# Kernel tuning notes

Hardware: AMD Instinct MI355X
Metric: run time of the kernel (lower is better)

Reference implementation:

```python
import jax, jax.numpy as jnp
import numpy as np

B, H, N, P = 2, 8, 2048, 64   # batch, heads, seq, head_dim
M, D = 4, 256                 # sketch count, sketch feature dim


def setup_inputs() -> dict:
    key = jax.random.key(0)
    kq, kk, ks, kr = jax.random.split(key, 4)
    scale = P ** -0.5  # keep exp(QK) numerically tame, std(dot) ~= 1/8
    Q = jax.random.normal(kq, (B, H, N, P), dtype=jnp.float32) * scale
    K = jax.random.normal(kk, (B, H, N, P), dtype=jnp.float32) * scale
    # indices into the concatenated [Q;K] token axis of length 2N
    sketching_matrix = jax.random.randint(ks, (B, M, D), 0, 2 * N)
    # Rademacher random signs, broadcast over [b,h,2n] in the reduction
    random_sign = jnp.sign(jax.random.normal(kr, (M, D), dtype=jnp.float32))
    random_sign = jnp.where(random_sign == 0, 1.0, random_sign)
    return {"Q": Q, "K": K, "sketching_matrix": sketching_matrix,
            "random_sign": random_sign}


def reference(Q, K, sketching_matrix, random_sign):
    b, h, n, p = Q.shape
    X = jnp.concatenate([Q, K], axis=2)          # [b,h,2n,p]
    Xt = jnp.transpose(X, (0, 2, 1, 3))          # [b,2n,h,p]
    # gather sketched landmarks: [b,m,d,h,p] -> [b,h,m,d,p]
    XS = Xt[jnp.arange(b)[:, None, None], sketching_matrix]
    XS = jnp.transpose(XS, (0, 3, 1, 2, 4))
    # RS_SM accumulate branch: exp of inner products, random-sign reduce over m
    product = jnp.einsum('bhnp,bhmdp->bhnmd', X, XS)   # [b,h,2n,m,d]
    AS = jnp.einsum('bhnmd,md->bhnd', jnp.exp(product), random_sign)
    return AS.astype(Q.dtype)                    # [b,h,2n,d]
```

## Files before the change

kernel.cpp:

```cpp
#include <hip/hip_runtime.h>
#include <hip/hip_bf16.h>

typedef __attribute__((ext_vector_type(8))) short short8;
typedef __attribute__((ext_vector_type(4))) float f32x4;

namespace {
constexpr int Nc  = 2048;
constexpr int NXc = 4096;
constexpr int Pc  = 64;
constexpr int Mc  = 4;
constexpr int Dc  = 256;
constexpr int BH  = 16;
constexpr int LDW = 72;
constexpr float LOG2E = 1.4426950408889634f;
}

__device__ inline float fexp2(float x) {
#if __has_builtin(__builtin_amdgcn_exp2f)
  return __builtin_amdgcn_exp2f(x);
#else
  return exp2f(x);
#endif
}

__device__ inline unsigned int bfpack(float a, float b) {
  union { __hip_bfloat162 h; unsigned int u; } cv;
  cv.h = __float22bfloat162_rn(make_float2(a, b));
  return cv.u;
}

__global__ __launch_bounds__(256) void prepass_kernel(
    const float* __restrict__ Q, const float* __restrict__ K,
    const int* __restrict__ SK, __hip_bfloat16* __restrict__ Wb)
{
  const int t  = blockIdx.x * 256 + threadIdx.x;
  const int q  = t & 7;
  const int r  = t >> 3;
  const int bh = r >> 10;
  const int md = r & 1023;
  const int b  = bh >> 3;
  const int idx = SK[b * (Mc * Dc) + md];
  const float* src = (idx < Nc) ? (Q + ((size_t)bh * Nc + idx) * Pc)
                                : (K + ((size_t)bh * Nc + (idx - Nc)) * Pc);
  const f32x4* s4 = (const f32x4*)(src + q * 8);
  f32x4 f0 = s4[0], f1 = s4[1];
  uint4 u;
  u.x = bfpack(f0.x * LOG2E, f0.y * LOG2E);
  u.y = bfpack(f0.z * LOG2E, f0.w * LOG2E);
  u.z = bfpack(f1.x * LOG2E, f1.y * LOG2E);
  u.w = bfpack(f1.z * LOG2E, f1.w * LOG2E);
  *(uint4*)(Wb + (size_t)r * Pc + q * 8) = u;
}

__global__ __launch_bounds__(256, 4) void sketch_main(
    const float* __restrict__ Q, const float* __restrict__ K,
    const __hip_bfloat16* __restrict__ Wb,
    const float* __restrict__ SGN, float* __restrict__ OUT)
{
  __shared__ __hip_bfloat16 Ws[2][64][LDW];
  __shared__ float Ss[Mc * Dc];

  const int t    = threadIdx.x;
  const int lane = t & 63;
  const int wv   = t >> 6;
  const int brow = lane & 15;
  const int q    = lane >> 4;
  const int bh   = blockIdx.y;
  const int n0   = blockIdx.x * 64;

  for (int i = t; i < Mc * Dc; i += 256) Ss[i] = SGN[i];

  const int nrow = n0 + wv * 16 + brow;
  const float* xsrc = (n0 < Nc) ? (Q + ((size_t)bh * Nc + nrow) * Pc)
                                : (K + ((size_t)bh * Nc + (nrow - Nc)) * Pc);
  f32x4 x0 = *(const f32x4*)(xsrc + q * 8);
  f32x4 x1 = *(const f32x4*)(xsrc + q * 8 + 4);
  f32x4 x2 = *(const f32x4*)(xsrc + 32 + q * 8);
  f32x4 x3 = *(const f32x4*)(xsrc + 32 + q * 8 + 4);
  short8 bfr0, bfr1;
  {
    union { short8 s; uint4 u; } c0, c1;
    c0.u.x = bfpack(x0.x, x0.y); c0.u.y = bfpack(x0.z, x0.w);
    c0.u.z = bfpack(x1.x, x1.y); c0.u.w = bfpack(x1.z, x1.w);
    c1.u.x = bfpack(x2.x, x2.y); c1.u.y = bfpack(x2.z, x2.w);
    c1.u.z = bfpack(x3.x, x3.y); c1.u.w = bfpack(x3.z, x3.w);
    bfr0 = c0.s; bfr1 = c1.s;
  }

  const __hip_bfloat16* wbase = Wb + (size_t)bh * (Mc * Dc) * Pc;
  const int tr = t >> 2;
  const int tq = t & 3;

  auto crow = [](int p) { return (p & 3) * Dc + (p >> 2) * 64; };

  {
    const __hip_bfloat16* wp = wbase + (size_t)(crow(0) + tr) * Pc + tq * 16;
    uint4 wa = *(const uint4*)wp;
    uint4 wb = *(const uint4*)(wp + 8);
    *(uint4*)&Ws[0][tr][tq * 16]     = wa;
    *(uint4*)&Ws[0][tr][tq * 16 + 8] = wb;
  }
  __syncthreads();

  f32x4 AS[4];
  #pragma unroll
  for (int dt = 0; dt < 4; ++dt) AS[dt] = (f32x4){0.f, 0.f, 0.f, 0.f};

  for (int p = 0; p < 16; ++p) {
    const int pn = (p < 15) ? p + 1 : 15;
    const __hip_bfloat16* wp = wbase + (size_t)(crow(pn) + tr) * Pc + tq * 16;
    uint4 wa = *(const uint4*)wp;
    uint4 wb = *(const uint4*)(wp + 8);

    const int buf = p & 1;
    const int m   = p & 3;
    const int dc  = p >> 2;

    #pragma unroll
    for (int dt = 0; dt < 4; ++dt) {
      short8 a0 = *(const short8*)&Ws[buf][dt * 16 + brow][q * 8];
      short8 a1 = *(const short8*)&Ws[buf][dt * 16 + brow][32 + q * 8];
      f32x4 c = {0.f, 0.f, 0.f, 0.f};
      c = __builtin_amdgcn_mfma_f32_16x16x32_bf16(a0, bfr0, c, 0, 0, 0);
      c = __builtin_amdgcn_mfma_f32_16x16x32_bf16(a1, bfr1, c, 0, 0, 0);
      const f32x4 sg = *(const f32x4*)&Ss[m * Dc + dc * 64 + dt * 16 + q * 4];
      AS[dt].x = fmaf(sg.x, fexp2(c.x), AS[dt].x);
      AS[dt].y = fmaf(sg.y, fexp2(c.y), AS[dt].y);
      AS[dt].z = fmaf(sg.z, fexp2(c.z), AS[dt].z);
      AS[dt].w = fmaf(sg.w, fexp2(c.w), AS[dt].w);
    }

    if (m == 3) {
      float* orow = OUT + ((size_t)bh * NXc + nrow) * Dc + dc * 64 + q * 4;
      #pragma unroll
      for (int dt = 0; dt < 4; ++dt) {
        *(f32x4*)(orow + dt * 16) = AS[dt];
        AS[dt] = (f32x4){0.f, 0.f, 0.f, 0.f};
      }
    }

    *(uint4*)&Ws[buf ^ 1][tr][tq * 16]     = wa;
    *(uint4*)&Ws[buf ^ 1][tr][tq * 16 + 8] = wb;
    __syncthreads();
  }
}

extern "C" void kernel_launch(void* const* d_in, const int* in_sizes, int n_in,
                              void* d_out, int out_size, void* d_ws, size_t ws_size,
                              hipStream_t stream) {
  (void)in_sizes; (void)n_in; (void)out_size; (void)ws_size;
  const float* Q   = (const float*)d_in[0];
  const float* K   = (const float*)d_in[1];
  const int*   SK  = (const int*)d_in[2];
  const float* SGN = (const float*)d_in[3];
  float* OUT = (float*)d_out;

  __hip_bfloat16* Wb = (__hip_bfloat16*)d_ws;

  prepass_kernel<<<dim3(512), dim3(256), 0, stream>>>(Q, K, SK, Wb);
  sketch_main<<<dim3(NXc / 64, BH), dim3(256), 0, stream>>>(Q, K, Wb, SGN, OUT);
}
```

Measured before the change: 99.83 us.

## Keep sketch weights register-resident per wave and stream token tiles through them

```diff
diff --git a/kernel.cpp b/kernel.cpp
--- a/kernel.cpp
+++ b/kernel.cpp
@@ -11,7 +11,8 @@
 constexpr int Mc  = 4;
 constexpr int Dc  = 256;
 constexpr int BH  = 16;
-constexpr int LDW = 72;
+constexpr int NCHUNK = 128;
+constexpr int NT = NCHUNK / 16;
 constexpr float LOG2E = 1.4426950408889634f;
 }
 
@@ -52,96 +53,88 @@
   *(uint4*)(Wb + (size_t)r * Pc + q * 8) = u;
 }
 
-__global__ __launch_bounds__(256, 4) void sketch_main(
+__global__ __launch_bounds__(256, 2) void sketch_main(
     const float* __restrict__ Q, const float* __restrict__ K,
     const __hip_bfloat16* __restrict__ Wb,
     const float* __restrict__ SGN, float* __restrict__ OUT)
 {
-  __shared__ __hip_bfloat16 Ws[2][64][LDW];
-  __shared__ float Ss[Mc * Dc];
-
   const int t    = threadIdx.x;
   const int lane = t & 63;
   const int wv   = t >> 6;
   const int brow = lane & 15;
   const int q    = lane >> 4;
   const int bh   = blockIdx.y;
-  const int n0   = blockIdx.x * 64;
+  const int n0   = blockIdx.x * NCHUNK;
 
-  for (int i = t; i < Mc * Dc; i += 256) Ss[i] = SGN[i];
-
-  const int nrow = n0 + wv * 16 + brow;
-  const float* xsrc = (n0 < Nc) ? (Q + ((size_t)bh * Nc + nrow) * Pc)
-                                : (K + ((size_t)bh * Nc + (nrow - Nc)) * Pc);
-  f32x4 x0 = *(const f32x4*)(xsrc + q * 8);
-  f32x4 x1 = *(const f32x4*)(xsrc + q * 8 + 4);
-  f32x4 x2 = *(const f32x4*)(xsrc + 32 + q * 8);
-  f32x4 x3 = *(const f32x4*)(xsrc + 32 + q * 8 + 4);
-  short8 bfr0, bfr1;
+  short8 wf[4][4][2];
   {
-    union { short8 s; uint4 u; } c0, c1;
-    c0.u.x = bfpack(x0.x, x0.y); c0.u.y = bfpack(x0.z, x0.w);
-    c0.u.z = bfpack(x1.x, x1.y); c0.u.w = bfpack(x1.z, x1.w);
-    c1.u.x = bfpack(x2.x, x2.y); c1.u.y = bfpack(x2.z, x2.w);
-    c1.u.z = bfpack(x3.x, x3.y); c1.u.w = bfpack(x3.z, x3.w);
-    bfr0 = c0.s; bfr1 = c1.s;
+    const __hip_bfloat16* wbase =
+        Wb + ((size_t)bh * (Mc * Dc) + wv * 64 + brow) * Pc + q * 8;
+    #pragma unroll
+    for (int m = 0; m < 4; ++m) {
+      #pragma unroll
+      for (int dt = 0; dt < 4; ++dt) {
+        const __hip_bfloat16* wp = wbase + (size_t)(m * Dc + dt * 16) * Pc;
+        wf[m][dt][0] = *(const short8*)(wp);
+        wf[m][dt][1] = *(const short8*)(wp + 32);
+      }
+    }
   }
 
-  const __hip_bfloat16* wbase = Wb + (size_t)bh * (Mc * Dc) * Pc;
-  const int tr = t >> 2;
-  const int tq = t & 3;
-
-  auto crow = [](int p) { return (p & 3) * Dc + (p >> 2) * 64; };
-
-  {
-    const __hip_bfloat16* wp = wbase + (size_t)(crow(0) + tr) * Pc + tq * 16;
-    uint4 wa = *(const uint4*)wp;
-    uint4 wb = *(const uint4*)(wp + 8);
-    *(uint4*)&Ws[0][tr][tq * 16]     = wa;
-    *(uint4*)&Ws[0][tr][tq * 16 + 8] = wb;
-  }
-  __syncthreads();
-
-  f32x4 AS[4];
+  f32x4 sg[4][4];
   #pragma unroll
-  for (int dt = 0; dt < 4; ++dt) AS[dt] = (f32x4){0.f, 0.f, 0.f, 0.f};
-
-  for (int p = 0; p < 16; ++p) {
-    const int pn = (p < 15) ? p + 1 : 15;
-    const __hip_bfloat16* wp = wbase + (size_t)(crow(pn) + tr) * Pc + tq * 16;
-    uint4 wa = *(const uint4*)wp;
-    uint4 wb = *(const uint4*)(wp + 8);
-
-    const int buf = p & 1;
-    const int m   = p & 3;
-    const int dc  = p >> 2;
-
+  for (int m = 0; m < 4; ++m) {
     #pragma unroll
     for (int dt = 0; dt < 4; ++dt) {
-      short8 a0 = *(const short8*)&Ws[buf][dt * 16 + brow][q * 8];
-      short8 a1 = *(const short8*)&Ws[buf][dt * 16 + brow][32 + q * 8];
-      f32x4 c = {0.f, 0.f, 0.f, 0.f};
-      c = __builtin_amdgcn_mfma_f32_16x16x32_bf16(a0, bfr0, c, 0, 0, 0);
-      c = __builtin_amdgcn_mfma_f32_16x16x32_bf16(a1, bfr1, c, 0, 0, 0);
-      const f32x4 sg = *(const f32x4*)&Ss[m * Dc + dc * 64 + dt * 16 + q * 4];
-      AS[dt].x = fmaf(sg.x, fexp2(c.x), AS[dt].x);
-      AS[dt].y = fmaf(sg.y, fexp2(c.y), AS[dt].y);
-      AS[dt].z = fmaf(sg.z, fexp2(c.z), AS[dt].z);
-      AS[dt].w = fmaf(sg.w, fexp2(c.w), AS[dt].w);
+      sg[m][dt] = *(const f32x4*)(SGN + m * Dc + wv * 64 + dt * 16 + q * 4);
+    }
+  }
+
+  const float* xrow = ((n0 < Nc) ? (Q + ((size_t)bh * Nc + n0) * Pc)
+                                 : (K + ((size_t)bh * Nc + (n0 - Nc)) * Pc))
+                      + (size_t)brow * Pc + q * 8;
+  float* obase = OUT + ((size_t)bh * NXc + n0 + brow) * Dc + wv * 64 + q * 4;
+
+  f32x4 xa = *(const f32x4*)(xrow);
+  f32x4 xb = *(const f32x4*)(xrow + 4);
+  f32x4 xc = *(const f32x4*)(xrow + 32);
+  f32x4 xd = *(const f32x4*)(xrow + 36);
+
+  for (int it = 0; it < NT; ++it) {
+    short8 b0, b1;
+    {
+      union { short8 s; uint4 u; } c0, c1;
+      c0.u.x = bfpack(xa.x, xa.y); c0.u.y = bfpack(xa.z, xa.w);
+      c0.u.z = bfpack(xb.x, xb.y); c0.u.w = bfpack(xb.z, xb.w);
+      c1.u.x = bfpack(xc.x, xc.y); c1.u.y = bfpack(xc.z, xc.w);
+      c1.u.z = bfpack(xd.x, xd.y); c1.u.w = bfpack(xd.z, xd.w);
+      b0 = c0.s; b1 = c1.s;
+    }
+    if (it + 1 < NT) {
+      const float* xn = xrow + (size_t)(it + 1) * 16 * Pc;
+      xa = *(const f32x4*)(xn);
+      xb = *(const f32x4*)(xn + 4);
+      xc = *(const f32x4*)(xn + 32);
+      xd = *(const f32x4*)(xn + 36);
     }
 
-    if (m == 3) {
-      float* orow = OUT + ((size_t)bh * NXc + nrow) * Dc + dc * 64 + q * 4;
+    float* orow = obase + (size_t)it * 16 * Dc;
+    #pragma unroll
+    for (int dt = 0; dt < 4; ++dt) {
+      f32x4 acc = {0.f, 0.f, 0.f, 0.f};
       #pragma unroll
-      for (int dt = 0; dt < 4; ++dt) {
-        *(f32x4*)(orow + dt * 16) = AS[dt];
-        AS[dt] = (f32x4){0.f, 0.f, 0.f, 0.f};
+      for (int m = 0; m < 4; ++m) {
+        f32x4 c = {0.f, 0.f, 0.f, 0.f};
+        c = __builtin_amdgcn_mfma_f32_16x16x32_bf16(wf[m][dt][0], b0, c, 0, 0, 0);
+        c = __builtin_amdgcn_mfma_f32_16x16x32_bf16(wf[m][dt][1], b1, c, 0, 0, 0);
+        const f32x4 s = sg[m][dt];
+        acc.x = fmaf(s.x, fexp2(c.x), acc.x);
+        acc.y = fmaf(s.y, fexp2(c.y), acc.y);
+        acc.z = fmaf(s.z, fexp2(c.z), acc.z);
+        acc.w = fmaf(s.w, fexp2(c.w), acc.w);
       }
+      *(f32x4*)(orow + dt * 16) = acc;
     }
-
-    *(uint4*)&Ws[buf ^ 1][tr][tq * 16]     = wa;
-    *(uint4*)&Ws[buf ^ 1][tr][tq * 16 + 8] = wb;
-    __syncthreads();
   }
 }
 
@@ -158,5 +151,5 @@
   __hip_bfloat16* Wb = (__hip_bfloat16*)d_ws;
 
   prepass_kernel<<<dim3(512), dim3(256), 0, stream>>>(Q, K, SK, Wb);
-  sketch_main<<<dim3(NXc / 64, BH), dim3(256), 0, stream>>>(Q, K, Wb, SGN, OUT);
+  sketch_main<<<dim3(NXc / NCHUNK, BH), dim3(256), 0, stream>>>(Q, K, Wb, SGN, OUT);
 }
```

Result: slower. 111.0 us (+11.1%).
